# Performance work log

Hardware: AMD Instinct MI355X
Metric: run time of the kernel (lower is better)

The kernel has to match this reference:

```python
import jax, jax.numpy as jnp
import numpy as np

NUM_EMBEDDINGS = 4096
EMBEDDING_DIM = 4096
COMMITMENT_COST = 0.25


def setup_inputs() -> dict:
    key = jax.random.key(0)
    k_in, k_cb = jax.random.split(key)
    inputs = jax.random.normal(k_in, (16, 512, EMBEDDING_DIM), dtype=jnp.float32)
    bound = 1.0 / NUM_EMBEDDINGS
    codebook = jax.random.uniform(
        k_cb, (NUM_EMBEDDINGS, EMBEDDING_DIM), dtype=jnp.float32,
        minval=-bound, maxval=bound)
    return {"inputs": inputs, "codebook": codebook}


def reference(inputs, codebook):
    B, K, D = inputs.shape
    flat = inputs.reshape(-1, D)  # [N, D], N = B*K
    distances = (
        jnp.sum(flat * flat, axis=1, keepdims=True)
        + jnp.sum(codebook * codebook, axis=1)
        - 2.0 * jnp.matmul(flat, codebook.T)
    )  # [N, num_embeddings]
    encoding_indices = jnp.argmin(distances, axis=1)  # [N]
    quantized = codebook[encoding_indices].reshape(B, K, D)

    e_latent_loss = jnp.mean((jax.lax.stop_gradient(quantized) - inputs) ** 2)
    q_latent_loss = jnp.mean((quantized - jax.lax.stop_gradient(inputs)) ** 2)
    loss = q_latent_loss + COMMITMENT_COST * e_latent_loss

    # straight-through estimator
    quantized_st = inputs + jax.lax.stop_gradient(quantized - inputs)

    # perplexity: codebook usage entropy (scatter one-hot == bincount)
    N = flat.shape[0]
    counts = jnp.zeros((NUM_EMBEDDINGS,), jnp.float32).at[encoding_indices].add(1.0)
    avg_probs = counts / N
    perplexity = jnp.exp(-jnp.sum(avg_probs * jnp.log(avg_probs + 1e-10)))

    return quantized_st, loss, perplexity
```

## Files before the change

kernel.cpp:

```cpp
#include <hip/hip_runtime.h>
#include <hip/hip_bf16.h>
#include <stdint.h>

typedef unsigned int u32;
typedef unsigned char u8;
typedef unsigned long long u64;
typedef __attribute__((ext_vector_type(8))) int i32x8;
typedef __attribute__((ext_vector_type(4))) int i32x4;
typedef __attribute__((ext_vector_type(4))) float f32x4;

#define NROWS 8192
#define NCODES 4096
#define DIM 4096
#define BK 128
#define KSTEPS (DIM / BK)

#define OFF_A      0UL
#define OFF_B      33554432UL
#define OFF_NORMS  50331648UL
#define OFF_RN     50348032UL
#define OFF_AMIN   50380800UL
#define OFF_COUNTS 50446336UL

__device__ __forceinline__ void stage16(const void* g, void* l) {
  __builtin_amdgcn_global_load_lds(
      (const __attribute__((address_space(1))) u32*)g,
      (__attribute__((address_space(3))) u32*)l, 16, 0, 0);
}

__device__ __forceinline__ u32 f2fp8(float f) {
  u32 u = __float_as_uint(f);
  u32 sign = (u >> 24) & 0x80u;
  u32 mag = u & 0x7FFFFFFFu;
  if (mag > 0x43E00000u) mag = 0x43E00000u;
  u32 b;
  if (mag < 0x3C800000u) {
    b = (u32)__float2int_rn(__uint_as_float(mag) * 512.0f);
  } else {
    u32 m = mag + 0x7FFFFu + ((mag >> 20) & 1u);
    u32 e = (m >> 23) - 127u;
    b = (((e + 7u) << 3) | ((m >> 20) & 7u)) & 0x7Fu;
  }
  return sign | b;
}

__device__ __forceinline__ u32 pack4(float4 v) {
  return f2fp8(v.x) | (f2fp8(v.y) << 8) | (f2fp8(v.z) << 16) | (f2fp8(v.w) << 24);
}

__device__ __forceinline__ float waveRed(float s) {
#pragma unroll
  for (int off = 32; off > 0; off >>= 1) s += __shfl_down(s, off);
  return s;
}

__device__ __forceinline__ i32x8 comb(i32x4 lo, i32x4 hi) {
  i32x8 r;
  r[0] = lo[0]; r[1] = lo[1]; r[2] = lo[2]; r[3] = lo[3];
  r[4] = hi[0]; r[5] = hi[1]; r[6] = hi[2]; r[7] = hi[3];
  return r;
}

__global__ void k_init(u64* __restrict__ amin, u32* __restrict__ counts) {
  int t = blockIdx.x * 256 + threadIdx.x;
  if (t < NROWS) amin[t] = ~0ULL;
  if (t < NCODES) counts[t] = 0u;
}

__global__ void k_cvtA(const float4* __restrict__ in, u32* __restrict__ outA,
                       float* __restrict__ rn) {
  int r = blockIdx.x;
  const float4* src = in + (size_t)r * (DIM / 4);
  u32* dst = outA + (size_t)r * (DIM / 4);
  float s = 0.0f;
#pragma unroll
  for (int q = 0; q < 4; ++q) {
    int j = q * 256 + threadIdx.x;
    float4 v = src[j];
    s += v.x * v.x + v.y * v.y + v.z * v.z + v.w * v.w;
    dst[j] = pack4(v);
  }
  s = waveRed(s);
  __shared__ float red[4];
  int wid = threadIdx.x >> 6, lane = threadIdx.x & 63;
  if (lane == 0) red[wid] = s;
  __syncthreads();
  if (threadIdx.x == 0) rn[r] = red[0] + red[1] + red[2] + red[3];
}

__global__ void k_cvtB(const float* __restrict__ cb, u32* __restrict__ Bb,
                       float* __restrict__ norms) {
  int row = blockIdx.x;
  const float4* src = (const float4*)(cb + (size_t)row * DIM);
  u32* dst = Bb + (size_t)row * (DIM / 4);
  float s = 0.0f;
#pragma unroll
  for (int q = 0; q < 4; ++q) {
    int j = q * 256 + threadIdx.x;
    float4 v = src[j];
    s += v.x * v.x + v.y * v.y + v.z * v.z + v.w * v.w;
    float4 sv;
    sv.x = v.x * 4096.0f; sv.y = v.y * 4096.0f;
    sv.z = v.z * 4096.0f; sv.w = v.w * 4096.0f;
    dst[j] = pack4(sv);
  }
  s = waveRed(s);
  __shared__ float red[4];
  int wid = threadIdx.x >> 6, lane = threadIdx.x & 63;
  if (lane == 0) red[wid] = s;
  __syncthreads();
  if (threadIdx.x == 0) norms[row] = red[0] + red[1] + red[2] + red[3];
}

__launch_bounds__(256)
__global__ void k_gemm_argmin(const u8* __restrict__ A,
                              const u8* __restrict__ B,
                              const float* __restrict__ norms,
                              u64* __restrict__ amin) {
  __shared__ u8 As[128 * BK];
  __shared__ u8 Bs[128 * BK];

  const int bm = blockIdx.x;
  const int bn = blockIdx.y;
  const int tid = threadIdx.x;
  const int w = tid >> 6;
  const int lane = tid & 63;
  const int wr = w >> 1, wc = w & 1;
  const int g = lane >> 4, c = lane & 15;

  const size_t rowA0 = (size_t)bm * 128;
  const size_t rowB0 = (size_t)bn * 128;

  const int colb = (((tid & 7) ^ ((tid >> 3) & 7)) << 4);
  const int srow = tid >> 3;

  const int colo = (((2 * g) ^ (c & 7)) << 4);
  const int cohi = (((2 * g + 1) ^ (c & 7)) << 4);

  f32x4 acc[4][4] = {};

  for (int kt = 0; kt < KSTEPS; ++kt) {
    __syncthreads();
#pragma unroll
    for (int j = 0; j < 4; ++j) {
      int o = j * 4096 + tid * 16;
      int row = j * 32 + srow;
      stage16(A + (rowA0 + row) * DIM + (size_t)kt * BK + colb, (char*)As + o);
      stage16(B + (rowB0 + row) * DIM + (size_t)kt * BK + colb, (char*)Bs + o);
    }
    __syncthreads();

    i32x8 af[4], bv[4];
#pragma unroll
    for (int m = 0; m < 4; ++m) {
      int rowm = (wr * 64 + m * 16 + c) * BK;
      af[m] = comb(*(const i32x4*)&As[rowm + colo],
                   *(const i32x4*)&As[rowm + cohi]);
    }
#pragma unroll
    for (int n = 0; n < 4; ++n) {
      int rown = (wc * 64 + n * 16 + c) * BK;
      bv[n] = comb(*(const i32x4*)&Bs[rown + colo],
                   *(const i32x4*)&Bs[rown + cohi]);
    }
#pragma unroll
    for (int m = 0; m < 4; ++m)
#pragma unroll
      for (int n = 0; n < 4; ++n)
        acc[m][n] = __builtin_amdgcn_mfma_scale_f32_16x16x128_f8f6f4(
            af[m], bv[n], acc[m][n], 0, 0, 0, 0x7F7F7F7F, 0, 0x7F7F7F7F);
  }

  const int rowBase = bm * 128 + wr * 64;
  const int colBase = bn * 128 + wc * 64;
  float nr[4];
#pragma unroll
  for (int n = 0; n < 4; ++n) nr[n] = norms[colBase + n * 16 + c];

#pragma unroll
  for (int m = 0; m < 4; ++m) {
#pragma unroll
    for (int j = 0; j < 4; ++j) {
      u64 key = ~0ULL;
#pragma unroll
      for (int n = 0; n < 4; ++n) {
        float d = nr[n] - acc[m][n][j] * 4.8828125e-4f;
        u32 u = __float_as_uint(d);
        u = (u & 0x80000000u) ? ~u : (u | 0x80000000u);
        u64 k2 = ((u64)u << 32) | (u32)(colBase + n * 16 + c);
        if (k2 < key) key = k2;
      }
#pragma unroll
      for (int off = 1; off < 16; off <<= 1) {
        u64 o = __shfl_xor(key, off);
        if (o < key) key = o;
      }
      if (c == 0) atomicMin(&amin[rowBase + m * 16 + g * 4 + j], key);
    }
  }
}

__global__ void k_out(const float4* __restrict__ cb, const u64* __restrict__ amin,
                      float4* __restrict__ out, u32* __restrict__ counts) {
  int r = blockIdx.x;
  u32 idx = (u32)(amin[r] & 0xFFFFFFFFu);
  if (threadIdx.x == 0) atomicAdd(&counts[idx], 1u);
  const float4* crow = cb + (size_t)idx * (DIM / 4);
  float4* orow = out + (size_t)r * (DIM / 4);
#pragma unroll
  for (int q = 0; q < 4; ++q) {
    int j = q * 256 + threadIdx.x;
    orow[j] = crow[j];
  }
}

__global__ void k_final(const u32* __restrict__ counts, const u64* __restrict__ amin,
                        const float* __restrict__ rn, float* __restrict__ out) {
  float acc = 0.0f;
  for (int r = threadIdx.x; r < NROWS; r += 256) {
    u32 u = (u32)(amin[r] >> 32);
    u32 b = (u & 0x80000000u) ? (u & 0x7FFFFFFFu) : ~u;
    acc += __uint_as_float(b) + rn[r];
  }
  float ent = 0.0f;
  for (int i = threadIdx.x; i < NCODES; i += 256) {
    float p = (float)counts[i] * (1.0f / (float)NROWS);
    ent -= p * logf(p + 1e-10f);
  }
  acc = waveRed(acc);
  ent = waveRed(ent);
  __shared__ float ra[4], re[4];
  int wid = threadIdx.x >> 6, lane = threadIdx.x & 63;
  if (lane == 0) { ra[wid] = acc; re[wid] = ent; }
  __syncthreads();
  if (threadIdx.x == 0) {
    float sse = ra[0] + ra[1] + ra[2] + ra[3];
    float e = re[0] + re[1] + re[2] + re[3];
    out[(size_t)NROWS * DIM] = 1.25f * sse * (1.0f / (float)((size_t)NROWS * DIM));
    out[(size_t)NROWS * DIM + 1] = expf(e);
  }
}

extern "C" void kernel_launch(void* const* d_in, const int* in_sizes, int n_in,
                              void* d_out, int out_size, void* d_ws, size_t ws_size,
                              hipStream_t stream) {
  const float* d_inputs = (const float*)d_in[0];
  const float* d_cb = (const float*)d_in[1];
  float* out = (float*)d_out;
  char* ws = (char*)d_ws;

  u8* A = (u8*)(ws + OFF_A);
  u8* B = (u8*)(ws + OFF_B);
  float* norms = (float*)(ws + OFF_NORMS);
  float* rn = (float*)(ws + OFF_RN);
  u64* amin = (u64*)(ws + OFF_AMIN);
  u32* counts = (u32*)(ws + OFF_COUNTS);

  k_init<<<32, 256, 0, stream>>>(amin, counts);
  k_cvtA<<<NROWS, 256, 0, stream>>>((const float4*)d_inputs, (u32*)A, rn);
  k_cvtB<<<NCODES, 256, 0, stream>>>(d_cb, (u32*)B, norms);
  dim3 grid(NROWS / 128, NCODES / 128);
  k_gemm_argmin<<<grid, 256, 0, stream>>>(A, B, norms, amin);
  k_out<<<NROWS, 256, 0, stream>>>((const float4*)d_cb, amin, (float4*)out, counts);
  k_final<<<1, 256, 0, stream>>>(counts, amin, rn, out);
}
```

Before: 269.0 us.

## Double-buffer LDS tiles in FP8 GEMM to overlap global loads with MFMA

Doubles the shared-memory A/B tiles and prefetches the next K-step via global_load_lds while MFMAs run on the current buffer. This replaces two block barriers per iteration with one wait-plus-barrier at the end. The aim is to hide global memory latency behind matrix compute. It doubles LDS usage per block, which can lower occupancy.

```diff
diff --git a/kernel.cpp b/kernel.cpp
--- a/kernel.cpp
+++ b/kernel.cpp
@@ -117,8 +117,8 @@
                               const u8* __restrict__ B,
                               const float* __restrict__ norms,
                               u64* __restrict__ amin) {
-  __shared__ u8 As[128 * BK];
-  __shared__ u8 Bs[128 * BK];
+  __shared__ u8 As[2][128 * BK];
+  __shared__ u8 Bs[2][128 * BK];
 
   const int bm = blockIdx.x;
   const int bn = blockIdx.y;
@@ -133,35 +133,53 @@
 
   const int colb = (((tid & 7) ^ ((tid >> 3) & 7)) << 4);
   const int srow = tid >> 3;
+  const u8* gA = A + rowA0 * DIM + colb;
+  const u8* gB = B + rowB0 * DIM + colb;
 
   const int colo = (((2 * g) ^ (c & 7)) << 4);
   const int cohi = (((2 * g + 1) ^ (c & 7)) << 4);
 
   f32x4 acc[4][4] = {};
 
+#pragma unroll
+  for (int j = 0; j < 4; ++j) {
+    int o = j * 4096 + tid * 16;
+    int row = j * 32 + srow;
+    stage16(gA + (size_t)row * DIM, (char*)As[0] + o);
+    stage16(gB + (size_t)row * DIM, (char*)Bs[0] + o);
+  }
+  asm volatile("s_waitcnt vmcnt(0)" ::: "memory");
+  __builtin_amdgcn_s_barrier();
+  __builtin_amdgcn_sched_barrier(0);
+
+#pragma unroll 2
   for (int kt = 0; kt < KSTEPS; ++kt) {
-    __syncthreads();
-#pragma unroll
-    for (int j = 0; j < 4; ++j) {
-      int o = j * 4096 + tid * 16;
-      int row = j * 32 + srow;
-      stage16(A + (rowA0 + row) * DIM + (size_t)kt * BK + colb, (char*)As + o);
-      stage16(B + (rowB0 + row) * DIM + (size_t)kt * BK + colb, (char*)Bs + o);
-    }
-    __syncthreads();
+    const int cur = kt & 1;
+    if (kt + 1 < KSTEPS) {
+#pragma unroll
+      for (int j = 0; j < 4; ++j) {
+        int o = j * 4096 + tid * 16;
+        int row = j * 32 + srow;
+        stage16(gA + (size_t)row * DIM + (size_t)(kt + 1) * BK,
+                (char*)As[cur ^ 1] + o);
+        stage16(gB + (size_t)row * DIM + (size_t)(kt + 1) * BK,
+                (char*)Bs[cur ^ 1] + o);
+      }
+    }
+    __builtin_amdgcn_sched_barrier(0);
 
     i32x8 af[4], bv[4];
 #pragma unroll
     for (int m = 0; m < 4; ++m) {
       int rowm = (wr * 64 + m * 16 + c) * BK;
-      af[m] = comb(*(const i32x4*)&As[rowm + colo],
-                   *(const i32x4*)&As[rowm + cohi]);
+      af[m] = comb(*(const i32x4*)&As[cur][rowm + colo],
+                   *(const i32x4*)&As[cur][rowm + cohi]);
     }
 #pragma unroll
     for (int n = 0; n < 4; ++n) {
       int rown = (wc * 64 + n * 16 + c) * BK;
-      bv[n] = comb(*(const i32x4*)&Bs[rown + colo],
-                   *(const i32x4*)&Bs[rown + cohi]);
+      bv[n] = comb(*(const i32x4*)&Bs[cur][rown + colo],
+                   *(const i32x4*)&Bs[cur][rown + cohi]);
     }
 #pragma unroll
     for (int m = 0; m < 4; ++m)
@@ -169,6 +187,10 @@
       for (int n = 0; n < 4; ++n)
         acc[m][n] = __builtin_amdgcn_mfma_scale_f32_16x16x128_f8f6f4(
             af[m], bv[n], acc[m][n], 0, 0, 0, 0x7F7F7F7F, 0, 0x7F7F7F7F);
+
+    asm volatile("s_waitcnt vmcnt(0)" ::: "memory");
+    __builtin_amdgcn_s_barrier();
+    __builtin_amdgcn_sched_barrier(0);
   }
 
   const int rowBase = bm * 128 + wr * 64;
```

Measured after the change: 265.9 us. About the same (-1.1%).
